# Performance work log

Measured on AMD Instinct MI355X. Metric: run time of the kernel, lower is better.

The kernel has to match this reference:

```python
import jax, jax.numpy as jnp
import numpy as np

F_DIM = 256; L = 4; B = 1; H = 160; W = 160; FH = 1024; N = B * H * W

def _ln(x, w, b):
    mu = jnp.mean(x, -1, keepdims=True)
    var = jnp.mean(jnp.square(x - mu), -1, keepdims=True)
    return (x - mu) * jax.lax.rsqrt(var + 1e-5) * w + b

def _conv(x, w, b, groups=1, pad=0):
    y = jax.lax.conv_general_dilated(x, w, (1, 1), [(pad, pad), (pad, pad)],
                                     dimension_numbers=('NCHW', 'OIHW', 'NCHW'),
                                     feature_group_count=groups)
    return y + b[None, :, None, None]

def _wsilu(x):
    return jax.nn.sigmoid(4.0 * x) * x

def setup_inputs() -> dict:
    key = jax.random.key(0)
    ks = iter(jax.random.split(key, 40))
    nk = lambda: next(ks)
    s = 1.0 / np.sqrt(F_DIM).astype(np.float32)
    inp = {}
    inp['x'] = jax.random.normal(nk(), (B, 1, H, W), jnp.float32)
    inp['cin_w1'] = jax.random.normal(nk(), (F_DIM, 1, 1, 1), jnp.float32)
    inp['cin_b1'] = jnp.zeros((F_DIM,), jnp.float32)
    inp['cin_w2'] = jax.random.normal(nk(), (F_DIM, 1, 7, 7), jnp.float32) * 0.15
    inp['cin_b2'] = jnp.zeros((F_DIM,), jnp.float32)
    inp['ln0_w'] = jnp.ones((F_DIM,), jnp.float32); inp['ln0_b'] = jnp.zeros((F_DIM,), jnp.float32)
    inp['ln1_w'] = jnp.ones((L, F_DIM), jnp.float32); inp['ln1_b'] = jnp.zeros((L, F_DIM), jnp.float32)
    inp['ln2_w'] = jnp.ones((L, F_DIM), jnp.float32); inp['ln2_b'] = jnp.zeros((L, F_DIM), jnp.float32)
    for n in ['att_tmk', 'att_tmv', 'att_tmr', 'ffn_tmk', 'ffn_tmr']:
        inp[n] = jax.random.uniform(nk(), (L, F_DIM), jnp.float32)
    inp['att_tf'] = jax.random.normal(nk(), (L, F_DIM), jnp.float32) * 0.5
    # time_decay is stored as -exp(raw) by the module's loader
    inp['att_td'] = -jnp.exp(jax.random.normal(nk(), (L, F_DIM), jnp.float32) * 0.5)
    for n in ['att_kw', 'att_vw', 'att_rw', 'att_ow', 'ffn_rw']:
        inp[n] = jax.random.normal(nk(), (L, F_DIM, F_DIM), jnp.float32) * s
    inp['ffn_kw'] = jax.random.normal(nk(), (L, FH, F_DIM), jnp.float32) * s
    inp['ffn_vw'] = jax.random.normal(nk(), (L, F_DIM, FH), jnp.float32) * (1.0 / np.sqrt(FH).astype(np.float32))
    inp['spa_dw_w'] = jax.random.normal(nk(), (L, F_DIM, 1, 7, 7), jnp.float32) * 0.15
    inp['spa_dw_b'] = jnp.zeros((L, F_DIM), jnp.float32)
    inp['spa_pw_w'] = jax.random.normal(nk(), (L, F_DIM, F_DIM, 1, 1), jnp.float32) * s
    inp['spa_pw_b'] = jnp.zeros((L, F_DIM), jnp.float32)
    st = jnp.zeros((5 * L, N, F_DIM), jnp.float32)
    st = st.at[4::5].add(-1e30)  # pp slots start at -1e30 as in torch init
    inp['state0'] = st
    return inp

def reference(x, cin_w1, cin_b1, cin_w2, cin_b2, ln0_w, ln0_b, ln1_w, ln1_b,
              ln2_w, ln2_b, att_tmk, att_tmv, att_tmr, att_tf, att_td,
              att_kw, att_vw, att_rw, att_ow, ffn_tmk, ffn_tmr, ffn_kw,
              ffn_vw, ffn_rw, spa_dw_w, spa_dw_b, spa_pw_w, spa_pw_b, state0):
    # conv stem: 1x1 -> depthwise 7x7 -> WSiLU
    d = _conv(x, cin_w1, cin_b1)
    d = _wsilu(_conv(d, cin_w2, cin_b2, groups=F_DIM, pad=3))
    d = d.transpose(0, 2, 3, 1).reshape(N, F_DIM)  # 'b f h w -> (b h w) f'
    for i in range(L):
        if i == 0:
            d = _ln(d, ln0_w, ln0_b)
        # --- SA: single-step RWKV WKV ---
        xs = _ln(d, ln1_w[i], ln1_b[i])
        sp = state0[5 * i + 1]
        aa = state0[5 * i + 2]; bb = state0[5 * i + 3]; pp = state0[5 * i + 4]
        xk = xs * att_tmk[i] + sp * (1 - att_tmk[i])
        xv = xs * att_tmv[i] + sp * (1 - att_tmv[i])
        xr = xs * att_tmr[i] + sp * (1 - att_tmr[i])
        r = jax.nn.sigmoid(xr @ att_rw[i].T)
        k = xk @ att_kw[i].T
        v = xv @ att_vw[i].T
        ww = att_tf[i] + k
        p = jnp.maximum(pp, ww)
        e1 = jnp.exp(pp - p); e2 = jnp.exp(ww - p)
        wkv = (e1 * aa + e2 * v) / (e1 * bb + e2)
        d = d + (r * wkv) @ att_ow[i].T
        # --- FF: squared-relu channel mix ---
        xs = _ln(d, ln2_w[i], ln2_b[i])
        sp = state0[5 * i + 0]
        xk = xs * ffn_tmk[i] + sp * (1 - ffn_tmk[i])
        xr = xs * ffn_tmr[i] + sp * (1 - ffn_tmr[i])
        rr = jax.nn.sigmoid(xr @ ffn_rw[i].T)
        kk = jnp.square(jax.nn.relu(xk @ ffn_kw[i].T))
        d = d + rr * (kk @ ffn_vw[i].T)
        # --- spatial residual block ---
        img = d.reshape(B, H, W, F_DIM).transpose(0, 3, 1, 2)
        img = img + _conv(_conv(img, spa_dw_w[i], spa_dw_b[i], groups=F_DIM, pad=3),
                          spa_pw_w[i], spa_pw_b[i])
        d = img.transpose(0, 2, 3, 1).reshape(N, F_DIM)
    return d.reshape(B, H, W, F_DIM).transpose(0, 3, 1, 2)
```

## Files before the change

### kernel.cpp

```cpp
#include <hip/hip_runtime.h>
#include <hip/hip_bf16.h>
#include <cstdint>
#include <cstddef>

#define F_DIMC 256
#define FHC    1024
#define IMGH   160
#define IMGW   160
#define NTOK   25600
#define NLAY   4

using bf16 = __hip_bfloat16;
typedef __attribute__((ext_vector_type(8))) short bf16x8;
typedef __attribute__((ext_vector_type(4))) float f32x4;

struct Cvt6 { const float* s[6]; bf16* d[6]; };
__global__ void cvt6_k(Cvt6 a, int n) {
    int z = blockIdx.y;
    int i = blockIdx.x * 256 + threadIdx.x;
    if (i < n) a.d[z][i] = __float2bfloat16(a.s[z][i]);
}
struct Cvt2 { const float* s[2]; bf16* d[2]; };
__global__ void cvt2_k(Cvt2 a, int n) {
    int z = blockIdx.y;
    int i = blockIdx.x * 256 + threadIdx.x;
    if (i < n) a.d[z][i] = __float2bfloat16(a.s[z][i]);
}

__global__ void dw_transpose_k(const float* __restrict__ src, float* __restrict__ dst, int n) {
    int i = blockIdx.x * 256 + threadIdx.x;
    if (i < n) {
        int f = i & (F_DIMC - 1);
        int lt = i >> 8;
        int t = lt % 49;
        int l = lt / 49;
        dst[i] = src[((size_t)l * F_DIMC + f) * 49 + t];
    }
}

__global__ __launch_bounds__(256)
void stem2_k(const float* __restrict__ x, const float* __restrict__ w1,
             const float* __restrict__ b1, const float* __restrict__ w2,
             const float* __restrict__ b2, float* __restrict__ d)
{
    __shared__ float wts[49][64];
    __shared__ float w1s[64], b1s[64], b2s[64];
    __shared__ float2 xp[7][22];
    const int tid = threadIdx.x;
    const int f0 = blockIdx.y * 64;
    const int y = blockIdx.x / 10;
    const int x0 = (blockIdx.x % 10) * 16;

    for (int idx = tid; idx < 49 * 64; idx += 256) {
        int t = idx >> 6, fl = idx & 63;
        wts[t][fl] = w2[(f0 + fl) * 49 + t];
    }
    if (tid < 64) {
        w1s[tid] = w1[f0 + tid];
        b1s[tid] = b1[f0 + tid];
        b2s[tid] = b2[f0 + tid];
    }
    for (int p = tid; p < 7 * 22; p += 256) {
        int py = p / 22, px = p % 22;
        int gy = y + py - 3, gx = x0 + px - 3;
        bool ok = (unsigned)gy < IMGH && (unsigned)gx < IMGW;
        xp[py][px] = ok ? make_float2(x[gy * IMGW + gx], 1.f) : make_float2(0.f, 0.f);
    }
    __syncthreads();

    const int fl = tid & 63;
    const int xbase = (tid >> 6) * 4;
    float acc[4] = {0.f, 0.f, 0.f, 0.f}, accw[4] = {0.f, 0.f, 0.f, 0.f};
    #pragma unroll
    for (int ky = 0; ky < 7; ++ky) {
        float2 row[10];
        #pragma unroll
        for (int q = 0; q < 10; ++q) row[q] = xp[ky][xbase + q];
        #pragma unroll
        for (int kx = 0; kx < 7; ++kx) {
            float w = wts[ky * 7 + kx][fl];
            #pragma unroll
            for (int j = 0; j < 4; ++j) {
                acc[j]  = fmaf(row[j + kx].x, w, acc[j]);
                accw[j] = fmaf(row[j + kx].y, w, accw[j]);
            }
        }
    }
    const float w1f = w1s[fl], b1f = b1s[fl], b2f = b2s[fl];
    #pragma unroll
    for (int j = 0; j < 4; ++j) {
        float u = fmaf(w1f, acc[j], fmaf(b1f, accw[j], b2f));
        int pix = y * IMGW + x0 + xbase + j;
        d[(size_t)pix * F_DIMC + f0 + fl] = u / (1.f + __expf(-4.f * u));
    }
}

__device__ __forceinline__ void wave_ln(float* x, const float* __restrict__ w,
                                        const float* __restrict__ b, int lane)
{
    float s = x[0] + x[1] + x[2] + x[3];
    #pragma unroll
    for (int m = 1; m < 64; m <<= 1) s += __shfl_xor(s, m, 64);
    float mu = s * 0.00390625f;
    float t0 = x[0] - mu, t1 = x[1] - mu, t2 = x[2] - mu, t3 = x[3] - mu;
    float v = t0 * t0 + t1 * t1 + t2 * t2 + t3 * t3;
    #pragma unroll
    for (int m = 1; m < 64; m <<= 1) v += __shfl_xor(v, m, 64);
    float inv = rsqrtf(v * 0.00390625f + 1e-5f);
    f32x4 wv = *(const f32x4*)(w + lane * 4);
    f32x4 bv = *(const f32x4*)(b + lane * 4);
    x[0] = t0 * inv * wv[0] + bv[0];
    x[1] = t1 * inv * wv[1] + bv[1];
    x[2] = t2 * inv * wv[2] + bv[2];
    x[3] = t3 * inv * wv[3] + bv[3];
}

union Pack4 { bf16 h[4]; uint2 u; };

template<bool LN0>
__global__ __launch_bounds__(256)
void lnmix_sa_k(float* __restrict__ d, const float* __restrict__ sp,
                const float* __restrict__ ln0w, const float* __restrict__ ln0b,
                const float* __restrict__ lnw, const float* __restrict__ lnb,
                const float* __restrict__ tmk, const float* __restrict__ tmv,
                const float* __restrict__ tmr,
                bf16* __restrict__ xk, bf16* __restrict__ xv, bf16* __restrict__ xr)
{
    const int lane = threadIdx.x & 63;
    const int n = blockIdx.x * 4 + (threadIdx.x >> 6);
    const int base = n * F_DIMC + lane * 4;
    f32x4 dv = *(const f32x4*)(d + base);
    float xo[4] = {dv[0], dv[1], dv[2], dv[3]};
    if (LN0) {
        wave_ln(xo, ln0w, ln0b, lane);
        f32x4 o = {xo[0], xo[1], xo[2], xo[3]};
        *(f32x4*)(d + base) = o;
    }
    float xs[4] = {xo[0], xo[1], xo[2], xo[3]};
    wave_ln(xs, lnw, lnb, lane);
    f32x4 spv = *(const f32x4*)(sp + base);
    f32x4 k4 = *(const f32x4*)(tmk + lane * 4);
    f32x4 v4 = *(const f32x4*)(tmv + lane * 4);
    f32x4 r4 = *(const f32x4*)(tmr + lane * 4);
    Pack4 pk, pv, pr;
    #pragma unroll
    for (int j = 0; j < 4; ++j) {
        pk.h[j] = __float2bfloat16(xs[j] * k4[j] + spv[j] * (1.f - k4[j]));
        pv.h[j] = __float2bfloat16(xs[j] * v4[j] + spv[j] * (1.f - v4[j]));
        pr.h[j] = __float2bfloat16(xs[j] * r4[j] + spv[j] * (1.f - r4[j]));
    }
    *(uint2*)(xk + base) = pk.u;
    *(uint2*)(xv + base) = pv.u;
    *(uint2*)(xr + base) = pr.u;
}

__global__ __launch_bounds__(256)
void lnmix_ff_k(const float* __restrict__ d, const float* __restrict__ sp,
                const float* __restrict__ lnw, const float* __restrict__ lnb,
                const float* __restrict__ tmk, const float* __restrict__ tmr,
                bf16* __restrict__ xk, bf16* __restrict__ xr)
{
    const int lane = threadIdx.x & 63;
    const int n = blockIdx.x * 4 + (threadIdx.x >> 6);
    const int base = n * F_DIMC + lane * 4;
    f32x4 dv = *(const f32x4*)(d + base);
    float xs[4] = {dv[0], dv[1], dv[2], dv[3]};
    wave_ln(xs, lnw, lnb, lane);
    f32x4 spv = *(const f32x4*)(sp + base);
    f32x4 k4 = *(const f32x4*)(tmk + lane * 4);
    f32x4 r4 = *(const f32x4*)(tmr + lane * 4);
    Pack4 pk, pr;
    #pragma unroll
    for (int j = 0; j < 4; ++j) {
        pk.h[j] = __float2bfloat16(xs[j] * k4[j] + spv[j] * (1.f - k4[j]));
        pr.h[j] = __float2bfloat16(xs[j] * r4[j] + spv[j] * (1.f - r4[j]));
    }
    *(uint2*)(xk + base) = pk.u;
    *(uint2*)(xr + base) = pr.u;
}

__global__ __launch_bounds__(256)
void wkv_k(const float* __restrict__ r_, const float* __restrict__ k_,
           const float* __restrict__ v_, const float* __restrict__ aa,
           const float* __restrict__ bb, const float* __restrict__ pp,
           const float* __restrict__ tf, bf16* __restrict__ out)
{
    int i = blockIdx.x * 256 + threadIdx.x;
    int f0 = (i << 2) & (F_DIMC - 1);
    f32x4 r4 = *(const f32x4*)(r_ + (size_t)i * 4);
    f32x4 k4 = *(const f32x4*)(k_ + (size_t)i * 4);
    f32x4 v4 = *(const f32x4*)(v_ + (size_t)i * 4);
    f32x4 a4 = *(const f32x4*)(aa + (size_t)i * 4);
    f32x4 b4 = *(const f32x4*)(bb + (size_t)i * 4);
    f32x4 p4 = *(const f32x4*)(pp + (size_t)i * 4);
    f32x4 t4 = *(const f32x4*)(tf + f0);
    Pack4 po;
    #pragma unroll
    for (int j = 0; j < 4; ++j) {
        float ww = t4[j] + k4[j];
        float p = fmaxf(p4[j], ww);
        float e1 = __expf(p4[j] - p);
        float e2 = __expf(ww - p);
        float wkv = (e1 * a4[j] + e2 * v4[j]) / (e1 * b4[j] + e2);
        po.h[j] = __float2bfloat16(r4[j] * wkv);
    }
    *(uint2*)(out + (size_t)i * 4) = po.u;
}

__global__ __launch_bounds__(256)
void dwconv_k(const float* __restrict__ d, const float* __restrict__ wT,
              const float* __restrict__ bias, bf16* __restrict__ out)
{
    __shared__ float patch[100 * 64];
    __shared__ float wt[49 * 64];
    const int lane = threadIdx.x;
    const int ty = threadIdx.y;
    const int f0 = blockIdx.z * 64;
    const int w0 = blockIdx.x * 4, h0 = blockIdx.y * 4;
    for (int t = ty; t < 49; t += 4) wt[t * 64 + lane] = wT[t * F_DIMC + f0 + lane];
    for (int p = ty; p < 100; p += 4) {
        int py = p / 10, px = p % 10;
        int gy = h0 + py - 3, gx = w0 + px - 3;
        float v = 0.f;
        if ((unsigned)gy < IMGH && (unsigned)gx < IMGW)
            v = d[(size_t)(gy * IMGW + gx) * F_DIMC + f0 + lane];
        patch[p * 64 + lane] = v;
    }
    __syncthreads();
    const float b = bias[f0 + lane];
    for (int pi = ty; pi < 16; pi += 4) {
        int py = pi >> 2, px = pi & 3;
        float acc = b;
        #pragma unroll
        for (int t = 0; t < 49; ++t) {
            int ky = t / 7, kx = t % 7;
            acc += patch[((py + ky) * 10 + (px + kx)) * 64 + lane] * wt[t * 64 + lane];
        }
        out[(size_t)((h0 + py) * IMGW + (w0 + px)) * F_DIMC + f0 + lane] = __float2bfloat16(acc);
    }
}

#define GEMM_BK 64

struct G3 { const bf16* A0; const bf16* A1; const bf16* A2;
            const bf16* W0; const bf16* W1; const bf16* W2;
            float* C0; float* C1; float* C2; };
__global__ __launch_bounds__(256)
void gemm3_k(G3 g)
{
    __shared__ __align__(16) bf16 As[128 * GEMM_BK];
    __shared__ __align__(16) bf16 Bs[128 * GEMM_BK];
    const int z = blockIdx.z;
    const bf16* __restrict__ A  = z == 0 ? g.A0 : z == 1 ? g.A1 : g.A2;
    const bf16* __restrict__ Bw = z == 0 ? g.W0 : z == 1 ? g.W1 : g.W2;
    float* __restrict__ C       = z == 0 ? g.C0 : z == 1 ? g.C1 : g.C2;
    const int tid = threadIdx.x;
    const int m0 = blockIdx.x * 128;
    const int n0 = blockIdx.y * 128;
    const int lane = tid & 63;
    const int wave = tid >> 6;
    const int wr = wave >> 1, wc = wave & 1;
    f32x4 acc[4][4];
    #pragma unroll
    for (int m = 0; m < 4; ++m)
        #pragma unroll
        for (int n = 0; n < 4; ++n) acc[m][n] = (f32x4){0.f, 0.f, 0.f, 0.f};

    for (int k0 = 0; k0 < F_DIMC; k0 += GEMM_BK) {
        #pragma unroll
        for (int s = 0; s < 4; ++s) {
            int e = s * 2048 + tid * 8;
            int row = e >> 6, col = e & 63;
            __builtin_amdgcn_global_load_lds(
                (const __attribute__((address_space(1))) void*)(A + (size_t)(m0 + row) * F_DIMC + (k0 + col)),
                (__attribute__((address_space(3))) void*)(&As[e]), 16, 0, 0);
        }
        #pragma unroll
        for (int s = 0; s < 4; ++s) {
            int e = s * 2048 + tid * 8;
            int row = e >> 6, col = e & 63;
            __builtin_amdgcn_global_load_lds(
                (const __attribute__((address_space(1))) void*)(Bw + (size_t)(n0 + row) * F_DIMC + (k0 + col)),
                (__attribute__((address_space(3))) void*)(&Bs[e]), 16, 0, 0);
        }
        __syncthreads();
        #pragma unroll
        for (int kk = 0; kk < GEMM_BK; kk += 32) {
            const int lr = lane & 15;
            const int lk = kk + (lane >> 4) * 8;
            bf16x8 af[4], bfr[4];
            #pragma unroll
            for (int m = 0; m < 4; ++m)
                af[m] = *(const bf16x8*)&As[(wr * 64 + m * 16 + lr) * GEMM_BK + lk];
            #pragma unroll
            for (int n = 0; n < 4; ++n)
                bfr[n] = *(const bf16x8*)&Bs[(wc * 64 + n * 16 + lr) * GEMM_BK + lk];
            #pragma unroll
            for (int m = 0; m < 4; ++m)
                #pragma unroll
                for (int n = 0; n < 4; ++n)
                    acc[m][n] = __builtin_amdgcn_mfma_f32_16x16x32_bf16(af[m], bfr[n], acc[m][n], 0, 0, 0);
        }
        __syncthreads();
    }
    const int lr0 = (lane >> 4) * 4;
    const int lc = lane & 15;
    #pragma unroll
    for (int m = 0; m < 4; ++m)
        #pragma unroll
        for (int n = 0; n < 4; ++n)
            #pragma unroll
            for (int j = 0; j < 4; ++j) {
                int row = m0 + wr * 64 + m * 16 + lr0 + j;
                int col = n0 + wc * 64 + n * 16 + lc;
                float v = acc[m][n][j];
                if (z == 2) v = 1.f / (1.f + __expf(-v));
                C[(size_t)row * F_DIMC + col] = v;
            }
}

template<int EPI>
__global__ __launch_bounds__(256)
void gemm_bt(const bf16* __restrict__ A, const bf16* __restrict__ Bw,
             int K, int Nout,
             float* __restrict__ Cf, bf16* __restrict__ Cb,
             const float* __restrict__ aux, const float* __restrict__ bias)
{
    __shared__ __align__(16) bf16 As[128 * GEMM_BK];
    __shared__ __align__(16) bf16 Bs[128 * GEMM_BK];
    const int tid = threadIdx.x;
    const int m0 = blockIdx.x * 128;
    const int n0 = blockIdx.y * 128;
    const int lane = tid & 63;
    const int wave = tid >> 6;
    const int wr = wave >> 1, wc = wave & 1;
    f32x4 acc[4][4];
    #pragma unroll
    for (int m = 0; m < 4; ++m)
        #pragma unroll
        for (int n = 0; n < 4; ++n) acc[m][n] = (f32x4){0.f, 0.f, 0.f, 0.f};

    for (int k0 = 0; k0 < K; k0 += GEMM_BK) {
        #pragma unroll
        for (int s = 0; s < 4; ++s) {
            int e = s * 2048 + tid * 8;
            int row = e >> 6, col = e & 63;
            __builtin_amdgcn_global_load_lds(
                (const __attribute__((address_space(1))) void*)(A + (size_t)(m0 + row) * K + (k0 + col)),
                (__attribute__((address_space(3))) void*)(&As[e]), 16, 0, 0);
        }
        #pragma unroll
        for (int s = 0; s < 4; ++s) {
            int e = s * 2048 + tid * 8;
            int row = e >> 6, col = e & 63;
            __builtin_amdgcn_global_load_lds(
                (const __attribute__((address_space(1))) void*)(Bw + (size_t)(n0 + row) * K + (k0 + col)),
                (__attribute__((address_space(3))) void*)(&Bs[e]), 16, 0, 0);
        }
        __syncthreads();
        #pragma unroll
        for (int kk = 0; kk < GEMM_BK; kk += 32) {
            const int lr = lane & 15;
            const int lk = kk + (lane >> 4) * 8;
            bf16x8 af[4], bfr[4];
            #pragma unroll
            for (int m = 0; m < 4; ++m)
                af[m] = *(const bf16x8*)&As[(wr * 64 + m * 16 + lr) * GEMM_BK + lk];
            #pragma unroll
            for (int n = 0; n < 4; ++n)
                bfr[n] = *(const bf16x8*)&Bs[(wc * 64 + n * 16 + lr) * GEMM_BK + lk];
            #pragma unroll
            for (int m = 0; m < 4; ++m)
                #pragma unroll
                for (int n = 0; n < 4; ++n)
                    acc[m][n] = __builtin_amdgcn_mfma_f32_16x16x32_bf16(af[m], bfr[n], acc[m][n], 0, 0, 0);
        }
        __syncthreads();
    }
    const int lr0 = (lane >> 4) * 4;
    const int lc = lane & 15;
    #pragma unroll
    for (int m = 0; m < 4; ++m) {
        #pragma unroll
        for (int n = 0; n < 4; ++n) {
            #pragma unroll
            for (int j = 0; j < 4; ++j) {
                int row = m0 + wr * 64 + m * 16 + lr0 + j;
                int col = n0 + wc * 64 + n * 16 + lc;
                size_t cidx = (size_t)row * Nout + col;
                float v = acc[m][n][j];
                if constexpr (EPI == 1) Cf[cidx] = 1.f / (1.f + __expf(-v));
                else if constexpr (EPI == 2) { float t = fmaxf(v, 0.f); Cb[cidx] = __float2bfloat16(t * t); }
                else if constexpr (EPI == 3) Cf[cidx] += v;
                else if constexpr (EPI == 4) Cf[cidx] += aux[cidx] * v;
                else if constexpr (EPI == 5) Cf[cidx] += v + bias[col];
            }
        }
    }
}

__global__ __launch_bounds__(256)
void transpose_out_k(const float* __restrict__ d, float* __restrict__ out)
{
    __shared__ float tile[32][33];
    const int n0 = blockIdx.x * 32, f0 = blockIdx.y * 32;
    const int tx = threadIdx.x, ty = threadIdx.y;
    for (int r = ty; r < 32; r += 8) tile[r][tx] = d[(size_t)(n0 + r) * F_DIMC + f0 + tx];
    __syncthreads();
    for (int r = ty; r < 32; r += 8) out[(size_t)(f0 + r) * NTOK + n0 + tx] = tile[tx][r];
}

extern "C" void kernel_launch(void* const* d_in, const int* in_sizes, int n_in,
                              void* d_out, int out_size, void* d_ws, size_t ws_size,
                              hipStream_t stream)
{
    if (n_in < 30) return;
    const float* x        = (const float*)d_in[0];
    const float* cin_w1   = (const float*)d_in[1];
    const float* cin_b1   = (const float*)d_in[2];
    const float* cin_w2   = (const float*)d_in[3];
    const float* cin_b2   = (const float*)d_in[4];
    const float* ln0_w    = (const float*)d_in[5];
    const float* ln0_b    = (const float*)d_in[6];
    const float* ln1_w    = (const float*)d_in[7];
    const float* ln1_b    = (const float*)d_in[8];
    const float* ln2_w    = (const float*)d_in[9];
    const float* ln2_b    = (const float*)d_in[10];
    const float* att_tmk  = (const float*)d_in[11];
    const float* att_tmv  = (const float*)d_in[12];
    const float* att_tmr  = (const float*)d_in[13];
    const float* ffn_tmk  = (const float*)d_in[14];
    const float* ffn_tmr  = (const float*)d_in[15];
    const float* att_tf   = (const float*)d_in[16];
    const float* att_kw   = (const float*)d_in[18];
    const float* att_vw   = (const float*)d_in[19];
    const float* att_rw   = (const float*)d_in[20];
    const float* att_ow   = (const float*)d_in[21];
    const float* ffn_rw   = (const float*)d_in[22];
    const float* ffn_kw   = (const float*)d_in[23];
    const float* ffn_vw   = (const float*)d_in[24];
    const float* spa_dw_w = (const float*)d_in[25];
    const float* spa_dw_b = (const float*)d_in[26];
    const float* spa_pw_w = (const float*)d_in[27];
    const float* spa_pw_b = (const float*)d_in[28];
    const float* state0   = (const float*)d_in[29];
    float* out = (float*)d_out;

    const size_t NF = (size_t)NTOK * F_DIMC;
    char* wsp = (char*)d_ws;
    size_t off = 0;
    auto alloc = [&](size_t bytes) -> void* {
        void* p = wsp + off;
        off += (bytes + 255) & ~(size_t)255;
        return p;
    };
    float* d_buf = (float*)alloc(NF * 4);
    float* Gk    = (float*)alloc(NF * 4);
    float* Gv    = (float*)alloc(NF * 4);
    float* Gr    = (float*)alloc(NF * 4);
    bf16*  xk    = (bf16*)alloc(NF * 2);
    bf16*  xv    = (bf16*)alloc(NF * 2);
    bf16*  xr    = (bf16*)alloc(NF * 2);
    bf16*  ab    = (bf16*)alloc(NF * 2);
    bf16*  kkb   = (bf16*)alloc((size_t)NTOK * FHC * 2);
    const size_t WSQ = (size_t)NLAY * F_DIMC * F_DIMC;
    bf16* kwb  = (bf16*)alloc(WSQ * 2);
    bf16* vwb  = (bf16*)alloc(WSQ * 2);
    bf16* rwb  = (bf16*)alloc(WSQ * 2);
    bf16* owb  = (bf16*)alloc(WSQ * 2);
    bf16* frwb = (bf16*)alloc(WSQ * 2);
    bf16* fkwb = (bf16*)alloc((size_t)NLAY * FHC * F_DIMC * 2);
    bf16* fvwb = (bf16*)alloc((size_t)NLAY * F_DIMC * FHC * 2);
    bf16* pwb  = (bf16*)alloc(WSQ * 2);
    float* dwT = (float*)alloc((size_t)NLAY * 49 * F_DIMC * 4);
    if (off > ws_size) return;

    {
        Cvt6 c6;
        c6.s[0] = att_kw;  c6.d[0] = kwb;
        c6.s[1] = att_vw;  c6.d[1] = vwb;
        c6.s[2] = att_rw;  c6.d[2] = rwb;
        c6.s[3] = att_ow;  c6.d[3] = owb;
        c6.s[4] = ffn_rw;  c6.d[4] = frwb;
        c6.s[5] = spa_pw_w; c6.d[5] = pwb;
        cvt6_k<<<dim3(((int)WSQ + 255) / 256, 6), dim3(256), 0, stream>>>(c6, (int)WSQ);
        Cvt2 c2;
        c2.s[0] = ffn_kw; c2.d[0] = fkwb;
        c2.s[1] = ffn_vw; c2.d[1] = fvwb;
        int n2 = NLAY * FHC * F_DIMC;
        cvt2_k<<<dim3((n2 + 255) / 256, 2), dim3(256), 0, stream>>>(c2, n2);
        int n = NLAY * 49 * F_DIMC;
        dw_transpose_k<<<dim3((n + 255) / 256), dim3(256), 0, stream>>>(spa_dw_w, dwT, n);
    }

    stem2_k<<<dim3(IMGH * 10, 4), dim3(256), 0, stream>>>(x, cin_w1, cin_b1, cin_w2, cin_b2, d_buf);

    for (int i = 0; i < NLAY; ++i) {
        const float* sp_ff = state0 + (size_t)(5 * i + 0) * NF;
        const float* sp_at = state0 + (size_t)(5 * i + 1) * NF;
        const float* aa    = state0 + (size_t)(5 * i + 2) * NF;
        const float* bb    = state0 + (size_t)(5 * i + 3) * NF;
        const float* pp    = state0 + (size_t)(5 * i + 4) * NF;
        const float* l1w = ln1_w + i * F_DIMC, *l1b = ln1_b + i * F_DIMC;
        const float* l2w = ln2_w + i * F_DIMC, *l2b = ln2_b + i * F_DIMC;
        const float* tmk = att_tmk + i * F_DIMC, *tmv = att_tmv + i * F_DIMC, *tmr = att_tmr + i * F_DIMC;
        const float* ftmk = ffn_tmk + i * F_DIMC, *ftmr = ffn_tmr + i * F_DIMC;
        const float* tf = att_tf + i * F_DIMC;
        const bf16* kw_i  = kwb  + (size_t)i * F_DIMC * F_DIMC;
        const bf16* vw_i  = vwb  + (size_t)i * F_DIMC * F_DIMC;
        const bf16* rw_i  = rwb  + (size_t)i * F_DIMC * F_DIMC;
        const bf16* ow_i  = owb  + (size_t)i * F_DIMC * F_DIMC;
        const bf16* frw_i = frwb + (size_t)i * F_DIMC * F_DIMC;
        const bf16* fkw_i = fkwb + (size_t)i * FHC * F_DIMC;
        const bf16* fvw_i = fvwb + (size_t)i * F_DIMC * FHC;
        const bf16* pw_i  = pwb  + (size_t)i * F_DIMC * F_DIMC;
        const float* dwT_i = dwT + (size_t)i * 49 * F_DIMC;
        const float* dwb_i = spa_dw_b + i * F_DIMC;
        const float* pwbias_i = spa_pw_b + i * F_DIMC;

        if (i == 0)
            lnmix_sa_k<true><<<dim3(NTOK / 4), dim3(256), 0, stream>>>(
                d_buf, sp_at, ln0_w, ln0_b, l1w, l1b, tmk, tmv, tmr, xk, xv, xr);
        else
            lnmix_sa_k<false><<<dim3(NTOK / 4), dim3(256), 0, stream>>>(
                d_buf, sp_at, ln0_w, ln0_b, l1w, l1b, tmk, tmv, tmr, xk, xv, xr);

        G3 g3;
        g3.A0 = xk; g3.A1 = xv; g3.A2 = xr;
        g3.W0 = kw_i; g3.W1 = vw_i; g3.W2 = rw_i;
        g3.C0 = Gk; g3.C1 = Gv; g3.C2 = Gr;
        gemm3_k<<<dim3(NTOK / 128, 2, 3), dim3(256), 0, stream>>>(g3);

        wkv_k<<<dim3((int)(NF / 4 / 256)), dim3(256), 0, stream>>>(Gr, Gk, Gv, aa, bb, pp, tf, ab);
        gemm_bt<3><<<dim3(NTOK / 128, 2), dim3(256), 0, stream>>>(ab, ow_i, F_DIMC, F_DIMC, d_buf, nullptr, nullptr, nullptr);

        lnmix_ff_k<<<dim3(NTOK / 4), dim3(256), 0, stream>>>(d_buf, sp_ff, l2w, l2b, ftmk, ftmr, xk, xr);
        gemm_bt<1><<<dim3(NTOK / 128, 2), dim3(256), 0, stream>>>(xr, frw_i, F_DIMC, F_DIMC, Gr, nullptr, nullptr, nullptr);
        gemm_bt<2><<<dim3(NTOK / 128, 8), dim3(256), 0, stream>>>(xk, fkw_i, F_DIMC, FHC, nullptr, kkb, nullptr, nullptr);
        gemm_bt<4><<<dim3(NTOK / 128, 2), dim3(256), 0, stream>>>(kkb, fvw_i, FHC, F_DIMC, d_buf, nullptr, Gr, nullptr);

        dwconv_k<<<dim3(IMGW / 4, IMGH / 4, 4), dim3(64, 4), 0, stream>>>(d_buf, dwT_i, dwb_i, ab);
        gemm_bt<5><<<dim3(NTOK / 128, 2), dim3(256), 0, stream>>>(ab, pw_i, F_DIMC, F_DIMC, d_buf, nullptr, nullptr, pwbias_i);
    }

    transpose_out_k<<<dim3(NTOK / 32, F_DIMC / 32), dim3(32, 8), 0, stream>>>(d_buf, out);
}
```

Before: 1.943 ms.

## Fuse KVR GEMMs with WKV, fuse FFN gate GEMM, swizzle LDS, enlarge dwconv tile

The three attention projections are now computed in one kernel whose epilogue applies the WKV recurrence step and sigmoid gate directly, removing the fp32 Gk/Gv/Gr intermediates and the separate wkv pass. The FFN receptance GEMM is fused into the value GEMM so the sigmoid gate is applied in registers rather than written and re-read. All GEMMs now use a 128-wide K tile with an XOR-swizzled LDS layout to avoid bank conflicts. The depthwise conv uses 8x8 output tiles with register row reuse. The trade-offs are more registers and LDS per block, which can lower occupancy, and 64x64 tiles with small per-wave work in the fused attention kernel.

```diff
diff --git a/kernel.cpp b/kernel.cpp
--- a/kernel.cpp
+++ b/kernel.cpp
@@ -13,6 +13,8 @@
 using bf16 = __hip_bfloat16;
 typedef __attribute__((ext_vector_type(8))) short bf16x8;
 typedef __attribute__((ext_vector_type(4))) float f32x4;
+
+#define MFMA16(a, b, c) __builtin_amdgcn_mfma_f32_16x16x32_bf16((a), (b), (c), 0, 0, 0)
 
 struct Cvt6 { const float* s[6]; bf16* d[6]; };
 __global__ void cvt6_k(Cvt6 a, int n) {
@@ -179,223 +181,297 @@
     *(uint2*)(xr + base) = pr.u;
 }
 
+
+__device__ __forceinline__ void stage_swz32(const bf16* __restrict__ g,
+                                            bf16* lds, int tid)
+{
+    #pragma unroll
+    for (int s = 0; s < 8; ++s) {
+        int chunk = s * 256 + tid;
+        int row = chunk >> 5, c16 = chunk & 31;
+        int gc = c16 ^ (row & 15);
+        __builtin_amdgcn_global_load_lds(
+            (const __attribute__((address_space(1))) void*)(g + (size_t)row * 256 + gc * 8),
+            (__attribute__((address_space(3))) void*)(lds + chunk * 8), 16, 0, 0);
+    }
+}
+
+__device__ __forceinline__ void stage_swz16(const bf16* __restrict__ g, int lda,
+                                            bf16* lds, int tid)
+{
+    #pragma unroll
+    for (int s = 0; s < 8; ++s) {
+        int chunk = s * 256 + tid;
+        int row = chunk >> 4, c16 = chunk & 15;
+        int gc = c16 ^ (row & 15);
+        __builtin_amdgcn_global_load_lds(
+            (const __attribute__((address_space(1))) void*)(g + (size_t)row * lda + gc * 8),
+            (__attribute__((address_space(3))) void*)(lds + chunk * 8), 16, 0, 0);
+    }
+}
+
+template<int RB>
+__device__ __forceinline__ bf16x8 frag_ld(const bf16* lds, int row, int cb)
+{
+    return *(const bf16x8*)((const char*)lds + row * RB + (cb ^ ((row & 15) << 4)));
+}
+
+__device__ __forceinline__ void pass64(const bf16* __restrict__ Ag, const bf16* __restrict__ Bg,
+                                       bf16* As, bf16* Bs, int tid, int wr, int wc,
+                                       int lr, int hi, f32x4 (&acc)[2][2])
+{
+    stage_swz32(Ag, As, tid);
+    stage_swz32(Bg, Bs, tid);
+    __syncthreads();
+    #pragma unroll
+    for (int ks = 0; ks < 8; ++ks) {
+        int cb = ks * 64 + hi * 16;
+        bf16x8 a0 = frag_ld<512>(As, wr * 32 + lr, cb);
+        bf16x8 a1 = frag_ld<512>(As, wr * 32 + 16 + lr, cb);
+        bf16x8 b0 = frag_ld<512>(Bs, wc * 32 + lr, cb);
+        bf16x8 b1 = frag_ld<512>(Bs, wc * 32 + 16 + lr, cb);
+        acc[0][0] = MFMA16(a0, b0, acc[0][0]);
+        acc[0][1] = MFMA16(a0, b1, acc[0][1]);
+        acc[1][0] = MFMA16(a1, b0, acc[1][0]);
+        acc[1][1] = MFMA16(a1, b1, acc[1][1]);
+    }
+    __syncthreads();
+}
+
+__global__ __launch_bounds__(256, 2)
+void sawkv_k(const bf16* __restrict__ xk, const bf16* __restrict__ xv,
+             const bf16* __restrict__ xr,
+             const bf16* __restrict__ kw, const bf16* __restrict__ vw,
+             const bf16* __restrict__ rw,
+             const float* __restrict__ aa, const float* __restrict__ bb,
+             const float* __restrict__ pp, const float* __restrict__ tf,
+             bf16* __restrict__ ab)
+{
+    __shared__ __align__(16) bf16 As[64 * 256];
+    __shared__ __align__(16) bf16 Bs[64 * 256];
+    const int tid = threadIdx.x, lane = tid & 63, wave = tid >> 6;
+    const int wr = wave >> 1, wc = wave & 1;
+    const int lr = lane & 15, hi = lane >> 4;
+    const int m0 = blockIdx.x * 64, n0 = blockIdx.y * 64;
+
+    f32x4 ak[2][2], av[2][2], ar[2][2];
+    #pragma unroll
+    for (int m = 0; m < 2; ++m)
+        #pragma unroll
+        for (int n = 0; n < 2; ++n) {
+            ak[m][n] = (f32x4){0.f, 0.f, 0.f, 0.f};
+            av[m][n] = (f32x4){0.f, 0.f, 0.f, 0.f};
+            ar[m][n] = (f32x4){0.f, 0.f, 0.f, 0.f};
+        }
+
+    pass64(xk + (size_t)m0 * 256, kw + (size_t)n0 * 256, As, Bs, tid, wr, wc, lr, hi, ak);
+    pass64(xv + (size_t)m0 * 256, vw + (size_t)n0 * 256, As, Bs, tid, wr, wc, lr, hi, av);
+    pass64(xr + (size_t)m0 * 256, rw + (size_t)n0 * 256, As, Bs, tid, wr, wc, lr, hi, ar);
+
+    const int lr0 = hi * 4;
+    #pragma unroll
+    for (int mf = 0; mf < 2; ++mf)
+        #pragma unroll
+        for (int nf = 0; nf < 2; ++nf) {
+            int col = n0 + wc * 32 + nf * 16 + lr;
+            float tfc = tf[col];
+            #pragma unroll
+            for (int j = 0; j < 4; ++j) {
+                int row = m0 + wr * 32 + mf * 16 + lr0 + j;
+                size_t idx = (size_t)row * F_DIMC + col;
+                float kk = ak[mf][nf][j], vv = av[mf][nf][j], rr = ar[mf][nf][j];
+                float P = pp[idx];
+                float ww = tfc + kk;
+                float p = fmaxf(P, ww);
+                float e1 = __expf(P - p), e2 = __expf(ww - p);
+                float wkv = (e1 * aa[idx] + e2 * vv) / (e1 * bb[idx] + e2);
+                ab[idx] = __float2bfloat16(wkv / (1.f + __expf(-rr)));
+            }
+        }
+}
+
+template<int EPI>
+__global__ __launch_bounds__(256, 2)
+void gemm128_k(const bf16* __restrict__ A, const bf16* __restrict__ Bw,
+               int lda, int ldb, int K, int Nout,
+               float* __restrict__ Cf, bf16* __restrict__ Cb,
+               const float* __restrict__ bias)
+{
+    __shared__ __align__(16) bf16 As[128 * 128];
+    __shared__ __align__(16) bf16 Bs[128 * 128];
+    const int tid = threadIdx.x, lane = tid & 63, wave = tid >> 6;
+    const int wr = wave >> 1, wc = wave & 1;
+    const int lr = lane & 15, hi = lane >> 4;
+    const int m0 = blockIdx.x * 128, n0 = blockIdx.y * 128;
+
+    f32x4 acc[4][4];
+    #pragma unroll
+    for (int m = 0; m < 4; ++m)
+        #pragma unroll
+        for (int n = 0; n < 4; ++n) acc[m][n] = (f32x4){0.f, 0.f, 0.f, 0.f};
+
+    for (int kt = 0; kt < K; kt += 128) {
+        stage_swz16(A + (size_t)m0 * lda + kt, lda, As, tid);
+        stage_swz16(Bw + (size_t)n0 * ldb + kt, ldb, Bs, tid);
+        __syncthreads();
+        #pragma unroll
+        for (int ks = 0; ks < 4; ++ks) {
+            int cb = ks * 64 + hi * 16;
+            bf16x8 a[4], b[4];
+            #pragma unroll
+            for (int mf = 0; mf < 4; ++mf) a[mf] = frag_ld<256>(As, wr * 64 + mf * 16 + lr, cb);
+            #pragma unroll
+            for (int nf = 0; nf < 4; ++nf) b[nf] = frag_ld<256>(Bs, wc * 64 + nf * 16 + lr, cb);
+            #pragma unroll
+            for (int mf = 0; mf < 4; ++mf)
+                #pragma unroll
+                for (int nf = 0; nf < 4; ++nf)
+                    acc[mf][nf] = MFMA16(a[mf], b[nf], acc[mf][nf]);
+        }
+        __syncthreads();
+    }
+
+    const int lr0 = hi * 4;
+    #pragma unroll
+    for (int mf = 0; mf < 4; ++mf)
+        #pragma unroll
+        for (int nf = 0; nf < 4; ++nf) {
+            int col = n0 + wc * 64 + nf * 16 + lr;
+            #pragma unroll
+            for (int j = 0; j < 4; ++j) {
+                int row = m0 + wr * 64 + mf * 16 + lr0 + j;
+                size_t cidx = (size_t)row * Nout + col;
+                float v = acc[mf][nf][j];
+                if constexpr (EPI == 2) { float t = fmaxf(v, 0.f); Cb[cidx] = __float2bfloat16(t * t); }
+                else if constexpr (EPI == 3) Cf[cidx] += v;
+                else if constexpr (EPI == 5) Cf[cidx] += v + bias[col];
+            }
+        }
+}
+
+__global__ __launch_bounds__(256, 2)
+void fvwrr_k(const bf16* __restrict__ kkb, const bf16* __restrict__ fvw,
+             const bf16* __restrict__ xr, const bf16* __restrict__ rw,
+             float* __restrict__ d)
+{
+    __shared__ __align__(16) bf16 As[128 * 128];
+    __shared__ __align__(16) bf16 Bs[128 * 128];
+    const int tid = threadIdx.x, lane = tid & 63, wave = tid >> 6;
+    const int wr = wave >> 1, wc = wave & 1;
+    const int lr = lane & 15, hi = lane >> 4;
+    const int m0 = blockIdx.x * 128, n0 = blockIdx.y * 128;
+
+    f32x4 arr[4][4], am[4][4];
+    #pragma unroll
+    for (int m = 0; m < 4; ++m)
+        #pragma unroll
+        for (int n = 0; n < 4; ++n) {
+            arr[m][n] = (f32x4){0.f, 0.f, 0.f, 0.f};
+            am[m][n]  = (f32x4){0.f, 0.f, 0.f, 0.f};
+        }
+
+    for (int kt = 0; kt < 256; kt += 128) {
+        stage_swz16(xr + (size_t)m0 * 256 + kt, 256, As, tid);
+        stage_swz16(rw + (size_t)n0 * 256 + kt, 256, Bs, tid);
+        __syncthreads();
+        #pragma unroll
+        for (int ks = 0; ks < 4; ++ks) {
+            int cb = ks * 64 + hi * 16;
+            bf16x8 a[4], b[4];
+            #pragma unroll
+            for (int mf = 0; mf < 4; ++mf) a[mf] = frag_ld<256>(As, wr * 64 + mf * 16 + lr, cb);
+            #pragma unroll
+            for (int nf = 0; nf < 4; ++nf) b[nf] = frag_ld<256>(Bs, wc * 64 + nf * 16 + lr, cb);
+            #pragma unroll
+            for (int mf = 0; mf < 4; ++mf)
+                #pragma unroll
+                for (int nf = 0; nf < 4; ++nf)
+                    arr[mf][nf] = MFMA16(a[mf], b[nf], arr[mf][nf]);
+        }
+        __syncthreads();
+    }
+    for (int kt = 0; kt < 1024; kt += 128) {
+        stage_swz16(kkb + (size_t)m0 * 1024 + kt, 1024, As, tid);
+        stage_swz16(fvw + (size_t)n0 * 1024 + kt, 1024, Bs, tid);
+        __syncthreads();
+        #pragma unroll
+        for (int ks = 0; ks < 4; ++ks) {
+            int cb = ks * 64 + hi * 16;
+            bf16x8 a[4], b[4];
+            #pragma unroll
+            for (int mf = 0; mf < 4; ++mf) a[mf] = frag_ld<256>(As, wr * 64 + mf * 16 + lr, cb);
+            #pragma unroll
+            for (int nf = 0; nf < 4; ++nf) b[nf] = frag_ld<256>(Bs, wc * 64 + nf * 16 + lr, cb);
+            #pragma unroll
+            for (int mf = 0; mf < 4; ++mf)
+                #pragma unroll
+                for (int nf = 0; nf < 4; ++nf)
+                    am[mf][nf] = MFMA16(a[mf], b[nf], am[mf][nf]);
+        }
+        __syncthreads();
+    }
+
+    const int lr0 = hi * 4;
+    #pragma unroll
+    for (int mf = 0; mf < 4; ++mf)
+        #pragma unroll
+        for (int nf = 0; nf < 4; ++nf) {
+            int col = n0 + wc * 64 + nf * 16 + lr;
+            #pragma unroll
+            for (int j = 0; j < 4; ++j) {
+                int row = m0 + wr * 64 + mf * 16 + lr0 + j;
+                size_t cidx = (size_t)row * F_DIMC + col;
+                float rr = 1.f / (1.f + __expf(-arr[mf][nf][j]));
+                d[cidx] += rr * am[mf][nf][j];
+            }
+        }
+}
+
 __global__ __launch_bounds__(256)
-void wkv_k(const float* __restrict__ r_, const float* __restrict__ k_,
-           const float* __restrict__ v_, const float* __restrict__ aa,
-           const float* __restrict__ bb, const float* __restrict__ pp,
-           const float* __restrict__ tf, bf16* __restrict__ out)
-{
-    int i = blockIdx.x * 256 + threadIdx.x;
-    int f0 = (i << 2) & (F_DIMC - 1);
-    f32x4 r4 = *(const f32x4*)(r_ + (size_t)i * 4);
-    f32x4 k4 = *(const f32x4*)(k_ + (size_t)i * 4);
-    f32x4 v4 = *(const f32x4*)(v_ + (size_t)i * 4);
-    f32x4 a4 = *(const f32x4*)(aa + (size_t)i * 4);
-    f32x4 b4 = *(const f32x4*)(bb + (size_t)i * 4);
-    f32x4 p4 = *(const f32x4*)(pp + (size_t)i * 4);
-    f32x4 t4 = *(const f32x4*)(tf + f0);
-    Pack4 po;
-    #pragma unroll
-    for (int j = 0; j < 4; ++j) {
-        float ww = t4[j] + k4[j];
-        float p = fmaxf(p4[j], ww);
-        float e1 = __expf(p4[j] - p);
-        float e2 = __expf(ww - p);
-        float wkv = (e1 * a4[j] + e2 * v4[j]) / (e1 * b4[j] + e2);
-        po.h[j] = __float2bfloat16(r4[j] * wkv);
-    }
-    *(uint2*)(out + (size_t)i * 4) = po.u;
-}
-
-__global__ __launch_bounds__(256)
-void dwconv_k(const float* __restrict__ d, const float* __restrict__ wT,
-              const float* __restrict__ bias, bf16* __restrict__ out)
-{
-    __shared__ float patch[100 * 64];
-    __shared__ float wt[49 * 64];
+void dwconv2_k(const float* __restrict__ d, const float* __restrict__ wT,
+               const float* __restrict__ bias, bf16* __restrict__ out)
+{
+    __shared__ float patch[196][64];
+    __shared__ float wt[49][64];
     const int lane = threadIdx.x;
     const int ty = threadIdx.y;
     const int f0 = blockIdx.z * 64;
-    const int w0 = blockIdx.x * 4, h0 = blockIdx.y * 4;
-    for (int t = ty; t < 49; t += 4) wt[t * 64 + lane] = wT[t * F_DIMC + f0 + lane];
-    for (int p = ty; p < 100; p += 4) {
-        int py = p / 10, px = p % 10;
+    const int w0 = blockIdx.x * 8, h0 = blockIdx.y * 8;
+
+    for (int t = ty; t < 49; t += 4) wt[t][lane] = wT[t * F_DIMC + f0 + lane];
+    for (int p = ty; p < 196; p += 4) {
+        int py = p / 14, px = p % 14;
         int gy = h0 + py - 3, gx = w0 + px - 3;
         float v = 0.f;
         if ((unsigned)gy < IMGH && (unsigned)gx < IMGW)
             v = d[(size_t)(gy * IMGW + gx) * F_DIMC + f0 + lane];
-        patch[p * 64 + lane] = v;
+        patch[p][lane] = v;
     }
     __syncthreads();
+
     const float b = bias[f0 + lane];
-    for (int pi = ty; pi < 16; pi += 4) {
-        int py = pi >> 2, px = pi & 3;
-        float acc = b;
-        #pragma unroll
-        for (int t = 0; t < 49; ++t) {
-            int ky = t / 7, kx = t % 7;
-            acc += patch[((py + ky) * 10 + (px + kx)) * 64 + lane] * wt[t * 64 + lane];
-        }
-        out[(size_t)((h0 + py) * IMGW + (w0 + px)) * F_DIMC + f0 + lane] = __float2bfloat16(acc);
-    }
-}
-
-#define GEMM_BK 64
-
-struct G3 { const bf16* A0; const bf16* A1; const bf16* A2;
-            const bf16* W0; const bf16* W1; const bf16* W2;
-            float* C0; float* C1; float* C2; };
-__global__ __launch_bounds__(256)
-void gemm3_k(G3 g)
-{
-    __shared__ __align__(16) bf16 As[128 * GEMM_BK];
-    __shared__ __align__(16) bf16 Bs[128 * GEMM_BK];
-    const int z = blockIdx.z;
-    const bf16* __restrict__ A  = z == 0 ? g.A0 : z == 1 ? g.A1 : g.A2;
-    const bf16* __restrict__ Bw = z == 0 ? g.W0 : z == 1 ? g.W1 : g.W2;
-    float* __restrict__ C       = z == 0 ? g.C0 : z == 1 ? g.C1 : g.C2;
-    const int tid = threadIdx.x;
-    const int m0 = blockIdx.x * 128;
-    const int n0 = blockIdx.y * 128;
-    const int lane = tid & 63;
-    const int wave = tid >> 6;
-    const int wr = wave >> 1, wc = wave & 1;
-    f32x4 acc[4][4];
-    #pragma unroll
-    for (int m = 0; m < 4; ++m)
-        #pragma unroll
-        for (int n = 0; n < 4; ++n) acc[m][n] = (f32x4){0.f, 0.f, 0.f, 0.f};
-
-    for (int k0 = 0; k0 < F_DIMC; k0 += GEMM_BK) {
-        #pragma unroll
-        for (int s = 0; s < 4; ++s) {
-            int e = s * 2048 + tid * 8;
-            int row = e >> 6, col = e & 63;
-            __builtin_amdgcn_global_load_lds(
-                (const __attribute__((address_space(1))) void*)(A + (size_t)(m0 + row) * F_DIMC + (k0 + col)),
-                (__attribute__((address_space(3))) void*)(&As[e]), 16, 0, 0);
-        }
-        #pragma unroll
-        for (int s = 0; s < 4; ++s) {
-            int e = s * 2048 + tid * 8;
-            int row = e >> 6, col = e & 63;
-            __builtin_amdgcn_global_load_lds(
-                (const __attribute__((address_space(1))) void*)(Bw + (size_t)(n0 + row) * F_DIMC + (k0 + col)),
-                (__attribute__((address_space(3))) void*)(&Bs[e]), 16, 0, 0);
-        }
-        __syncthreads();
-        #pragma unroll
-        for (int kk = 0; kk < GEMM_BK; kk += 32) {
-            const int lr = lane & 15;
-            const int lk = kk + (lane >> 4) * 8;
-            bf16x8 af[4], bfr[4];
-            #pragma unroll
-            for (int m = 0; m < 4; ++m)
-                af[m] = *(const bf16x8*)&As[(wr * 64 + m * 16 + lr) * GEMM_BK + lk];
-            #pragma unroll
-            for (int n = 0; n < 4; ++n)
-                bfr[n] = *(const bf16x8*)&Bs[(wc * 64 + n * 16 + lr) * GEMM_BK + lk];
-            #pragma unroll
-            for (int m = 0; m < 4; ++m)
+    #pragma unroll
+    for (int rr = 0; rr < 2; ++rr) {
+        int ry = ty * 2 + rr;
+        float acc8[8];
+        #pragma unroll
+        for (int px = 0; px < 8; ++px) acc8[px] = b;
+        #pragma unroll
+        for (int ky = 0; ky < 7; ++ky) {
+            float rowv[14];
+            #pragma unroll
+            for (int c = 0; c < 14; ++c) rowv[c] = patch[(ry + ky) * 14 + c][lane];
+            #pragma unroll
+            for (int kx = 0; kx < 7; ++kx) {
+                float w = wt[ky * 7 + kx][lane];
                 #pragma unroll
-                for (int n = 0; n < 4; ++n)
-                    acc[m][n] = __builtin_amdgcn_mfma_f32_16x16x32_bf16(af[m], bfr[n], acc[m][n], 0, 0, 0);
-        }
-        __syncthreads();
-    }
-    const int lr0 = (lane >> 4) * 4;
-    const int lc = lane & 15;
-    #pragma unroll
-    for (int m = 0; m < 4; ++m)
-        #pragma unroll
-        for (int n = 0; n < 4; ++n)
-            #pragma unroll
-            for (int j = 0; j < 4; ++j) {
-                int row = m0 + wr * 64 + m * 16 + lr0 + j;
-                int col = n0 + wc * 64 + n * 16 + lc;
-                float v = acc[m][n][j];
-                if (z == 2) v = 1.f / (1.f + __expf(-v));
-                C[(size_t)row * F_DIMC + col] = v;
+                for (int px = 0; px < 8; ++px)
+                    acc8[px] = fmaf(rowv[px + kx], w, acc8[px]);
             }
-}
-
-template<int EPI>
-__global__ __launch_bounds__(256)
-void gemm_bt(const bf16* __restrict__ A, const bf16* __restrict__ Bw,
-             int K, int Nout,
-             float* __restrict__ Cf, bf16* __restrict__ Cb,
-             const float* __restrict__ aux, const float* __restrict__ bias)
-{
-    __shared__ __align__(16) bf16 As[128 * GEMM_BK];
-    __shared__ __align__(16) bf16 Bs[128 * GEMM_BK];
-    const int tid = threadIdx.x;
-    const int m0 = blockIdx.x * 128;
-    const int n0 = blockIdx.y * 128;
-    const int lane = tid & 63;
-    const int wave = tid >> 6;
-    const int wr = wave >> 1, wc = wave & 1;
-    f32x4 acc[4][4];
-    #pragma unroll
-    for (int m = 0; m < 4; ++m)
-        #pragma unroll
-        for (int n = 0; n < 4; ++n) acc[m][n] = (f32x4){0.f, 0.f, 0.f, 0.f};
-
-    for (int k0 = 0; k0 < K; k0 += GEMM_BK) {
-        #pragma unroll
-        for (int s = 0; s < 4; ++s) {
-            int e = s * 2048 + tid * 8;
-            int row = e >> 6, col = e & 63;
-            __builtin_amdgcn_global_load_lds(
-                (const __attribute__((address_space(1))) void*)(A + (size_t)(m0 + row) * K + (k0 + col)),
-                (__attribute__((address_space(3))) void*)(&As[e]), 16, 0, 0);
-        }
-        #pragma unroll
-        for (int s = 0; s < 4; ++s) {
-            int e = s * 2048 + tid * 8;
-            int row = e >> 6, col = e & 63;
-            __builtin_amdgcn_global_load_lds(
-                (const __attribute__((address_space(1))) void*)(Bw + (size_t)(n0 + row) * K + (k0 + col)),
-                (__attribute__((address_space(3))) void*)(&Bs[e]), 16, 0, 0);
-        }
-        __syncthreads();
-        #pragma unroll
-        for (int kk = 0; kk < GEMM_BK; kk += 32) {
-            const int lr = lane & 15;
-            const int lk = kk + (lane >> 4) * 8;
-            bf16x8 af[4], bfr[4];
-            #pragma unroll
-            for (int m = 0; m < 4; ++m)
-                af[m] = *(const bf16x8*)&As[(wr * 64 + m * 16 + lr) * GEMM_BK + lk];
-            #pragma unroll
-            for (int n = 0; n < 4; ++n)
-                bfr[n] = *(const bf16x8*)&Bs[(wc * 64 + n * 16 + lr) * GEMM_BK + lk];
-            #pragma unroll
-            for (int m = 0; m < 4; ++m)
-                #pragma unroll
-                for (int n = 0; n < 4; ++n)
-                    acc[m][n] = __builtin_amdgcn_mfma_f32_16x16x32_bf16(af[m], bfr[n], acc[m][n], 0, 0, 0);
-        }
-        __syncthreads();
-    }
-    const int lr0 = (lane >> 4) * 4;
-    const int lc = lane & 15;
-    #pragma unroll
-    for (int m = 0; m < 4; ++m) {
-        #pragma unroll
-        for (int n = 0; n < 4; ++n) {
-            #pragma unroll
-            for (int j = 0; j < 4; ++j) {
-                int row = m0 + wr * 64 + m * 16 + lr0 + j;
-                int col = n0 + wc * 64 + n * 16 + lc;
-                size_t cidx = (size_t)row * Nout + col;
-                float v = acc[m][n][j];
-                if constexpr (EPI == 1) Cf[cidx] = 1.f / (1.f + __expf(-v));
-                else if constexpr (EPI == 2) { float t = fmaxf(v, 0.f); Cb[cidx] = __float2bfloat16(t * t); }
-                else if constexpr (EPI == 3) Cf[cidx] += v;
-                else if constexpr (EPI == 4) Cf[cidx] += aux[cidx] * v;
-                else if constexpr (EPI == 5) Cf[cidx] += v + bias[col];
-            }
-        }
+        }
+        #pragma unroll
+        for (int px = 0; px < 8; ++px)
+            out[(size_t)((h0 + ry) * IMGW + (w0 + px)) * F_DIMC + f0 + lane] = __float2bfloat16(acc8[px]);
     }
 }
 
@@ -455,9 +531,6 @@
         return p;
     };
     float* d_buf = (float*)alloc(NF * 4);
-    float* Gk    = (float*)alloc(NF * 4);
-    float* Gv    = (float*)alloc(NF * 4);
-    float* Gr    = (float*)alloc(NF * 4);
     bf16*  xk    = (bf16*)alloc(NF * 2);
     bf16*  xv    = (bf16*)alloc(NF * 2);
     bf16*  xr    = (bf16*)alloc(NF * 2);
@@ -525,22 +598,23 @@
             lnmix_sa_k<false><<<dim3(NTOK / 4), dim3(256), 0, stream>>>(
                 d_buf, sp_at, ln0_w, ln0_b, l1w, l1b, tmk, tmv, tmr, xk, xv, xr);
 
-        G3 g3;
-        g3.A0 = xk; g3.A1 = xv; g3.A2 = xr;
-        g3.W0 = kw_i; g3.W1 = vw_i; g3.W2 = rw_i;
-        g3.C0 = Gk; g3.C1 = Gv; g3.C2 = Gr;
-        gemm3_k<<<dim3(NTOK / 128, 2, 3), dim3(256), 0, stream>>>(g3);
-
-        wkv_k<<<dim3((int)(NF / 4 / 256)), dim3(256), 0, stream>>>(Gr, Gk, Gv, aa, bb, pp, tf, ab);
-        gemm_bt<3><<<dim3(NTOK / 128, 2), dim3(256), 0, stream>>>(ab, ow_i, F_DIMC, F_DIMC, d_buf, nullptr, nullptr, nullptr);
+        sawkv_k<<<dim3(NTOK / 64, 4), dim3(256), 0, stream>>>(
+            xk, xv, xr, kw_i, vw_i, rw_i, aa, bb, pp, tf, ab);
+
+        gemm128_k<3><<<dim3(NTOK / 128, 2), dim3(256), 0, stream>>>(
+            ab, ow_i, F_DIMC, F_DIMC, F_DIMC, F_DIMC, d_buf, nullptr, nullptr);
 
         lnmix_ff_k<<<dim3(NTOK / 4), dim3(256), 0, stream>>>(d_buf, sp_ff, l2w, l2b, ftmk, ftmr, xk, xr);
-        gemm_bt<1><<<dim3(NTOK / 128, 2), dim3(256), 0, stream>>>(xr, frw_i, F_DIMC, F_DIMC, Gr, nullptr, nullptr, nullptr);
-        gemm_bt<2><<<dim3(NTOK / 128, 8), dim3(256), 0, stream>>>(xk, fkw_i, F_DIMC, FHC, nullptr, kkb, nullptr, nullptr);
-        gemm_bt<4><<<dim3(NTOK / 128, 2), dim3(256), 0, stream>>>(kkb, fvw_i, FHC, F_DIMC, d_buf, nullptr, Gr, nullptr);
-
-        dwconv_k<<<dim3(IMGW / 4, IMGH / 4, 4), dim3(64, 4), 0, stream>>>(d_buf, dwT_i, dwb_i, ab);
-        gemm_bt<5><<<dim3(NTOK / 128, 2), dim3(256), 0, stream>>>(ab, pw_i, F_DIMC, F_DIMC, d_buf, nullptr, nullptr, pwbias_i);
+
+        gemm128_k<2><<<dim3(NTOK / 128, 8), dim3(256), 0, stream>>>(
+            xk, fkw_i, F_DIMC, F_DIMC, F_DIMC, FHC, nullptr, kkb, nullptr);
+
+        fvwrr_k<<<dim3(NTOK / 128, 2), dim3(256), 0, stream>>>(kkb, fvw_i, xr, frw_i, d_buf);
+
+        dwconv2_k<<<dim3(IMGW / 8, IMGH / 8, 4), dim3(64, 4), 0, stream>>>(d_buf, dwT_i, dwb_i, ab);
+
+        gemm128_k<5><<<dim3(NTOK / 128, 2), dim3(256), 0, stream>>>(
+            ab, pw_i, F_DIMC, F_DIMC, F_DIMC, F_DIMC, d_buf, nullptr, pwbias_i);
     }
 
     transpose_out_k<<<dim3(NTOK / 32, F_DIMC / 32), dim3(32, 8), 0, stream>>>(d_buf, out);
```

Result: no change. 1.952 ms (+0.4%).
